# Kernel optimization log

Hardware: AMD Instinct MI355X
Metric: run time of the kernel (lower is better)

Reference implementation:

```python
import jax, jax.numpy as jnp
import numpy as np
import math


def _rope_2d(k, height, width):
    """Additive 2D sinusoidal position embedding. k: (B, N, D), N == height*width."""
    B, N, D = k.shape
    d_half = D // 2
    y_idx = jnp.arange(height, dtype=jnp.float32) / max(height - 1, 1)
    x_idx = jnp.arange(width, dtype=jnp.float32) / max(width - 1, 1)
    y_grid, x_grid = jnp.meshgrid(y_idx, x_idx, indexing='ij')
    y_flat = y_grid.reshape(-1)  # (N,)
    x_flat = x_grid.reshape(-1)
    freq = jnp.exp(jnp.arange(0, d_half, 2, dtype=jnp.float32) * (-(math.log(10000.0) / d_half)))

    def pos_half(flat, scale):
        ang = flat[:, None] * freq[None, :] * scale  # (N, ceil(d_half/2))
        p = jnp.zeros((N, d_half), dtype=jnp.float32)
        p = p.at[:, 0::2].set(jnp.sin(ang))
        n_odd = p[:, 1::2].shape[-1]
        p = p.at[:, 1::2].set(jnp.cos(ang[:, :n_odd]))
        return p

    pos_emb = jnp.concatenate([pos_half(y_flat, float(height)), pos_half(x_flat, float(width))], axis=-1)
    if pos_emb.shape[-1] < D:
        pos_emb = jnp.pad(pos_emb, ((0, 0), (0, D - pos_emb.shape[-1])))
    elif pos_emb.shape[-1] > D:
        pos_emb = pos_emb[:, :D]
    return k + pos_emb[None]


def setup_inputs() -> dict:
    key = jax.random.key(0)
    k1, k2, k3, k4 = jax.random.split(key, 4)
    B, N, dim = 2, 4096, 768
    num_heads, key_dim = 2, 8
    # xavier-uniform-like scales
    sq = math.sqrt(6.0 / (dim + num_heads * (key_dim + 1)))
    sk = math.sqrt(6.0 / (dim + key_dim))
    return {
        'query_tokens': jax.random.normal(k1, (B, N, dim), dtype=jnp.float32),
        'key_tokens': jax.random.normal(k2, (B, N, dim), dtype=jnp.float32),
        'Wq': jax.random.uniform(k3, (dim, num_heads * (key_dim + 1)), minval=-sq, maxval=sq, dtype=jnp.float32),
        'Wk': jax.random.uniform(k4, (dim, key_dim), minval=-sk, maxval=sk, dtype=jnp.float32),
        'spatial_bias': jnp.zeros((1, 1, 1), dtype=jnp.float32),
        'height': 64,
        'width': 64,
    }


def reference(query_tokens, key_tokens, Wq, Wk, spatial_bias, height, width):
    key_dim = Wk.shape[-1]
    num_heads = Wq.shape[-1] // (key_dim + 1)
    scale = key_dim ** (-0.5)
    B, N_q, _ = query_tokens.shape
    qw = (query_tokens @ Wq).reshape(B, N_q, num_heads, key_dim + 1)
    q = qw[..., :key_dim]          # (B, Nq, H, d)
    w = qw[..., -1]                # (B, Nq, H)
    k = key_tokens @ Wk            # (B, Nk, d)
    if height is not None and width is not None:
        k = _rope_2d(k, height, width)
    scores = jax.nn.relu(jnp.einsum('bqhd,bkd->bhqk', q, k) * scale)  # (B,H,Nq,Nk)
    index_scores = jnp.einsum('bqh,bhqk->bqk', w, scores)
    return index_scores + spatial_bias
```

## Files before the change

### kernel.cpp

```cpp
#include <hip/hip_runtime.h>
#include <math.h>

#define BB 2
#define NN 4096
#define DIM 768
#define QSTRIDE 20

__global__ __launch_bounds__(256) void qproj_kernel(const float* __restrict__ x,
                                                    const float* __restrict__ Wq,
                                                    float* __restrict__ qd) {
  const int lane = threadIdx.x & 63;
  const int pair = blockIdx.x * 4 + (threadIdx.x >> 6);
  const int row0 = pair * 2;
  const float* xr0 = x + (size_t)row0 * DIM;
  const float* xr1 = xr0 + DIM;

  float acc0[18], acc1[18];
#pragma unroll
  for (int c = 0; c < 18; ++c) { acc0[c] = 0.f; acc1[c] = 0.f; }

#pragma unroll
  for (int j = 0; j < DIM / 64; ++j) {
    const int i = lane + 64 * j;
    const float x0 = xr0[i];
    const float x1 = xr1[i];
    const float* wr = Wq + i * 18;
#pragma unroll
    for (int c = 0; c < 9; ++c) {
      const float2 w2 = *(const float2*)(wr + 2 * c);
      acc0[2 * c]     = fmaf(x0, w2.x, acc0[2 * c]);
      acc0[2 * c + 1] = fmaf(x0, w2.y, acc0[2 * c + 1]);
      acc1[2 * c]     = fmaf(x1, w2.x, acc1[2 * c]);
      acc1[2 * c + 1] = fmaf(x1, w2.y, acc1[2 * c + 1]);
    }
  }

#pragma unroll
  for (int off = 32; off >= 1; off >>= 1) {
#pragma unroll
    for (int c = 0; c < 18; ++c) {
      acc0[c] += __shfl_xor(acc0[c], off, 64);
      acc1[c] += __shfl_xor(acc1[c], off, 64);
    }
  }

  const int r = lane >> 5;
  const int l = lane & 31;
  if (l < 18) {
    int src;
    if (l < 8) src = l;
    else if (l < 16) src = l + 1;
    else if (l == 16) src = 8;
    else src = 17;
    float v = r ? acc1[0] : acc0[0];
#pragma unroll
    for (int c = 1; c < 18; ++c) {
      const float cand = r ? acc1[c] : acc0[c];
      v = (src == c) ? cand : v;
    }
    qd[(size_t)(row0 + r) * QSTRIDE + l] = v;
  }
}

__global__ __launch_bounds__(256) void kproj_kernel(const float* __restrict__ x,
                                                    const float* __restrict__ Wk,
                                                    const int* __restrict__ hp,
                                                    const int* __restrict__ wp,
                                                    float* __restrict__ kd) {
  const int lane = threadIdx.x & 63;
  const int pair = blockIdx.x * 4 + (threadIdx.x >> 6);
  const int row0 = pair * 2;
  const float* xr0 = x + (size_t)row0 * DIM;
  const float* xr1 = xr0 + DIM;

  float acc0[8], acc1[8];
#pragma unroll
  for (int c = 0; c < 8; ++c) { acc0[c] = 0.f; acc1[c] = 0.f; }

#pragma unroll
  for (int j = 0; j < DIM / 64; ++j) {
    const int i = lane + 64 * j;
    const float x0 = xr0[i];
    const float x1 = xr1[i];
    const float4 wa = *(const float4*)(Wk + i * 8);
    const float4 wb = *(const float4*)(Wk + i * 8 + 4);
    acc0[0] = fmaf(x0, wa.x, acc0[0]); acc0[1] = fmaf(x0, wa.y, acc0[1]);
    acc0[2] = fmaf(x0, wa.z, acc0[2]); acc0[3] = fmaf(x0, wa.w, acc0[3]);
    acc0[4] = fmaf(x0, wb.x, acc0[4]); acc0[5] = fmaf(x0, wb.y, acc0[5]);
    acc0[6] = fmaf(x0, wb.z, acc0[6]); acc0[7] = fmaf(x0, wb.w, acc0[7]);
    acc1[0] = fmaf(x1, wa.x, acc1[0]); acc1[1] = fmaf(x1, wa.y, acc1[1]);
    acc1[2] = fmaf(x1, wa.z, acc1[2]); acc1[3] = fmaf(x1, wa.w, acc1[3]);
    acc1[4] = fmaf(x1, wb.x, acc1[4]); acc1[5] = fmaf(x1, wb.y, acc1[5]);
    acc1[6] = fmaf(x1, wb.z, acc1[6]); acc1[7] = fmaf(x1, wb.w, acc1[7]);
  }

#pragma unroll
  for (int off = 32; off >= 1; off >>= 1) {
#pragma unroll
    for (int c = 0; c < 8; ++c) {
      acc0[c] += __shfl_xor(acc0[c], off, 64);
      acc1[c] += __shfl_xor(acc1[c], off, 64);
    }
  }

  const int r = lane >> 5;
  const int l = lane & 31;
  if (l < 8) {
    const int row = row0 + r;
    const int h = hp[0];
    const int w = wp[0];
    const int n = row % NN;
    const int yi = n / w;
    const int xi = n - yi * w;
    const int hd = (h - 1) > 1 ? (h - 1) : 1;
    const int wd = (w - 1) > 1 ? (w - 1) : 1;
    const float yv = (float)yi / (float)hd;
    const float xv = (float)xi / (float)wd;
    const float base = (l < 4) ? yv : xv;
    const float sc = (l < 4) ? (float)h : (float)w;
    const float fr = (l & 2) ? 0.01f : 1.0f;
    const float ang = base * fr * sc;
    const float pe = (l & 1) ? cosf(ang) : sinf(ang);
    float v = r ? acc1[0] : acc0[0];
#pragma unroll
    for (int c = 1; c < 8; ++c) {
      const float cand = r ? acc1[c] : acc0[c];
      v = (l == c) ? cand : v;
    }
    kd[(size_t)row * 8 + l] = v + pe;
  }
}

__device__ __forceinline__ float dot8(const float4 a, const float4 b,
                                      const float* __restrict__ k8) {
  float d = a.x * k8[0];
  d = fmaf(a.y, k8[1], d);
  d = fmaf(a.z, k8[2], d);
  d = fmaf(a.w, k8[3], d);
  d = fmaf(b.x, k8[4], d);
  d = fmaf(b.y, k8[5], d);
  d = fmaf(b.z, k8[6], d);
  d = fmaf(b.w, k8[7], d);
  return d;
}

__global__ __launch_bounds__(256) void scores_kernel(const float* __restrict__ qd,
                                                     const float* __restrict__ kd,
                                                     const float* __restrict__ bias,
                                                     float* __restrict__ out) {
  __shared__ float ks[64 * 9];
  __shared__ float qs[32 * QSTRIDE];

  const int tid = threadIdx.x;
  const int kb = blockIdx.x;
  const int qb = blockIdx.y;
  const int b  = blockIdx.z;

  if (tid < 128) {
    const float4 v = ((const float4*)(kd + ((size_t)b * NN + kb * 64) * 8))[tid];
    const int key = tid >> 1;
    const int off = (tid & 1) * 4;
    float* dst = ks + key * 9 + off;
    dst[0] = v.x; dst[1] = v.y; dst[2] = v.z; dst[3] = v.w;
  }
  if (tid < 160) {
    ((float4*)qs)[tid] = ((const float4*)(qd + ((size_t)b * NN + qb * 32) * QSTRIDE))[tid];
  }
  __syncthreads();

  const int tx = tid & 15;
  const int ty = tid >> 4;
  const float sb = bias[0];
  const float scale = 0.35355339059327373f;

  const int k0 = tx * 4;
  float kv[4][8];
#pragma unroll
  for (int i = 0; i < 4; ++i) {
    const float* kp = ks + (k0 + i) * 9;
#pragma unroll
    for (int d = 0; d < 8; ++d) kv[i][d] = kp[d];
  }

#pragma unroll
  for (int qi = 0; qi < 2; ++qi) {
    const int lq = ty * 2 + qi;
    const float* qp = qs + lq * QSTRIDE;
    const float4 a0 = *(const float4*)(qp);
    const float4 a1 = *(const float4*)(qp + 4);
    const float4 b0 = *(const float4*)(qp + 8);
    const float4 b1 = *(const float4*)(qp + 12);
    const float w0 = qp[16];
    const float w1 = qp[17];

    float4 res;
    float* r = (float*)&res;
#pragma unroll
    for (int i = 0; i < 4; ++i) {
      float d0 = dot8(a0, a1, kv[i]);
      float d1 = dot8(b0, b1, kv[i]);
      d0 = fmaxf(d0 * scale, 0.f);
      d1 = fmaxf(d1 * scale, 0.f);
      r[i] = fmaf(w0, d0, fmaf(w1, d1, sb));
    }

    const int q = qb * 32 + lq;
    float* op = out + ((size_t)b * NN + q) * (size_t)NN + (size_t)(kb * 64 + k0);
    *(float4*)op = res;
  }
}

extern "C" void kernel_launch(void* const* d_in, const int* in_sizes, int n_in,
                              void* d_out, int out_size, void* d_ws, size_t ws_size,
                              hipStream_t stream) {
  const float* qt = (const float*)d_in[0];
  const float* kt = (const float*)d_in[1];
  const float* Wq = (const float*)d_in[2];
  const float* Wk = (const float*)d_in[3];
  const float* sb = (const float*)d_in[4];
  const int* hp = (const int*)d_in[5];
  const int* wp = (const int*)d_in[6];

  float* qd = (float*)d_ws;
  float* kd = qd + (size_t)BB * NN * QSTRIDE;
  float* outp = (float*)d_out;

  qproj_kernel<<<BB * NN / 8, 256, 0, stream>>>(qt, Wq, qd);
  kproj_kernel<<<BB * NN / 8, 256, 0, stream>>>(kt, Wk, hp, wp, kd);
  scores_kernel<<<dim3(64, NN / 32, BB), 256, 0, stream>>>(qd, kd, sb, outp);
}
```

Before: 203.8 us.

## Merge projection kernels, widen key tile to 128, use nontemporal output stores

Fuses the q and k projection kernels into one launch that uses a 2D grid, removing one kernel launch. The scores kernel's key tile grows from 64 to 128, so each thread computes 8 keys and halves the number of blocks. Outputs are written with two nontemporal 16-byte stores to stream the 128MB result past the cache. The larger tile raises per-thread register use.

```diff
diff --git a/kernel.cpp b/kernel.cpp
--- a/kernel.cpp
+++ b/kernel.cpp
@@ -5,129 +5,131 @@
 #define NN 4096
 #define DIM 768
 #define QSTRIDE 20
-
-__global__ __launch_bounds__(256) void qproj_kernel(const float* __restrict__ x,
-                                                    const float* __restrict__ Wq,
-                                                    float* __restrict__ qd) {
+#define KT 128
+
+typedef float f32x4 __attribute__((ext_vector_type(4)));
+
+__global__ __launch_bounds__(256) void proj_kernel(const float* __restrict__ xq,
+                                                   const float* __restrict__ Wq,
+                                                   float* __restrict__ qd,
+                                                   const float* __restrict__ xk,
+                                                   const float* __restrict__ Wk,
+                                                   const int* __restrict__ hp,
+                                                   const int* __restrict__ wp,
+                                                   float* __restrict__ kd) {
   const int lane = threadIdx.x & 63;
   const int pair = blockIdx.x * 4 + (threadIdx.x >> 6);
   const int row0 = pair * 2;
-  const float* xr0 = x + (size_t)row0 * DIM;
-  const float* xr1 = xr0 + DIM;
-
-  float acc0[18], acc1[18];
-#pragma unroll
-  for (int c = 0; c < 18; ++c) { acc0[c] = 0.f; acc1[c] = 0.f; }
-
-#pragma unroll
-  for (int j = 0; j < DIM / 64; ++j) {
-    const int i = lane + 64 * j;
-    const float x0 = xr0[i];
-    const float x1 = xr1[i];
-    const float* wr = Wq + i * 18;
-#pragma unroll
-    for (int c = 0; c < 9; ++c) {
-      const float2 w2 = *(const float2*)(wr + 2 * c);
-      acc0[2 * c]     = fmaf(x0, w2.x, acc0[2 * c]);
-      acc0[2 * c + 1] = fmaf(x0, w2.y, acc0[2 * c + 1]);
-      acc1[2 * c]     = fmaf(x1, w2.x, acc1[2 * c]);
-      acc1[2 * c + 1] = fmaf(x1, w2.y, acc1[2 * c + 1]);
-    }
-  }
-
-#pragma unroll
-  for (int off = 32; off >= 1; off >>= 1) {
-#pragma unroll
-    for (int c = 0; c < 18; ++c) {
-      acc0[c] += __shfl_xor(acc0[c], off, 64);
-      acc1[c] += __shfl_xor(acc1[c], off, 64);
-    }
-  }
-
-  const int r = lane >> 5;
-  const int l = lane & 31;
-  if (l < 18) {
-    int src;
-    if (l < 8) src = l;
-    else if (l < 16) src = l + 1;
-    else if (l == 16) src = 8;
-    else src = 17;
-    float v = r ? acc1[0] : acc0[0];
-#pragma unroll
-    for (int c = 1; c < 18; ++c) {
-      const float cand = r ? acc1[c] : acc0[c];
-      v = (src == c) ? cand : v;
-    }
-    qd[(size_t)(row0 + r) * QSTRIDE + l] = v;
-  }
-}
-
-__global__ __launch_bounds__(256) void kproj_kernel(const float* __restrict__ x,
-                                                    const float* __restrict__ Wk,
-                                                    const int* __restrict__ hp,
-                                                    const int* __restrict__ wp,
-                                                    float* __restrict__ kd) {
-  const int lane = threadIdx.x & 63;
-  const int pair = blockIdx.x * 4 + (threadIdx.x >> 6);
-  const int row0 = pair * 2;
-  const float* xr0 = x + (size_t)row0 * DIM;
-  const float* xr1 = xr0 + DIM;
-
-  float acc0[8], acc1[8];
-#pragma unroll
-  for (int c = 0; c < 8; ++c) { acc0[c] = 0.f; acc1[c] = 0.f; }
-
-#pragma unroll
-  for (int j = 0; j < DIM / 64; ++j) {
-    const int i = lane + 64 * j;
-    const float x0 = xr0[i];
-    const float x1 = xr1[i];
-    const float4 wa = *(const float4*)(Wk + i * 8);
-    const float4 wb = *(const float4*)(Wk + i * 8 + 4);
-    acc0[0] = fmaf(x0, wa.x, acc0[0]); acc0[1] = fmaf(x0, wa.y, acc0[1]);
-    acc0[2] = fmaf(x0, wa.z, acc0[2]); acc0[3] = fmaf(x0, wa.w, acc0[3]);
-    acc0[4] = fmaf(x0, wb.x, acc0[4]); acc0[5] = fmaf(x0, wb.y, acc0[5]);
-    acc0[6] = fmaf(x0, wb.z, acc0[6]); acc0[7] = fmaf(x0, wb.w, acc0[7]);
-    acc1[0] = fmaf(x1, wa.x, acc1[0]); acc1[1] = fmaf(x1, wa.y, acc1[1]);
-    acc1[2] = fmaf(x1, wa.z, acc1[2]); acc1[3] = fmaf(x1, wa.w, acc1[3]);
-    acc1[4] = fmaf(x1, wb.x, acc1[4]); acc1[5] = fmaf(x1, wb.y, acc1[5]);
-    acc1[6] = fmaf(x1, wb.z, acc1[6]); acc1[7] = fmaf(x1, wb.w, acc1[7]);
-  }
-
-#pragma unroll
-  for (int off = 32; off >= 1; off >>= 1) {
-#pragma unroll
-    for (int c = 0; c < 8; ++c) {
-      acc0[c] += __shfl_xor(acc0[c], off, 64);
-      acc1[c] += __shfl_xor(acc1[c], off, 64);
-    }
-  }
-
-  const int r = lane >> 5;
-  const int l = lane & 31;
-  if (l < 8) {
-    const int row = row0 + r;
-    const int h = hp[0];
-    const int w = wp[0];
-    const int n = row % NN;
-    const int yi = n / w;
-    const int xi = n - yi * w;
-    const int hd = (h - 1) > 1 ? (h - 1) : 1;
-    const int wd = (w - 1) > 1 ? (w - 1) : 1;
-    const float yv = (float)yi / (float)hd;
-    const float xv = (float)xi / (float)wd;
-    const float base = (l < 4) ? yv : xv;
-    const float sc = (l < 4) ? (float)h : (float)w;
-    const float fr = (l & 2) ? 0.01f : 1.0f;
-    const float ang = base * fr * sc;
-    const float pe = (l & 1) ? cosf(ang) : sinf(ang);
-    float v = r ? acc1[0] : acc0[0];
-#pragma unroll
-    for (int c = 1; c < 8; ++c) {
-      const float cand = r ? acc1[c] : acc0[c];
-      v = (l == c) ? cand : v;
-    }
-    kd[(size_t)row * 8 + l] = v + pe;
+
+  if (blockIdx.y == 0) {
+    const float* xr0 = xq + (size_t)row0 * DIM;
+    const float* xr1 = xr0 + DIM;
+
+    float acc0[18], acc1[18];
+#pragma unroll
+    for (int c = 0; c < 18; ++c) { acc0[c] = 0.f; acc1[c] = 0.f; }
+
+#pragma unroll
+    for (int j = 0; j < DIM / 64; ++j) {
+      const int i = lane + 64 * j;
+      const float x0 = xr0[i];
+      const float x1 = xr1[i];
+      const float* wr = Wq + i * 18;
+#pragma unroll
+      for (int c = 0; c < 9; ++c) {
+        const float2 w2 = *(const float2*)(wr + 2 * c);
+        acc0[2 * c]     = fmaf(x0, w2.x, acc0[2 * c]);
+        acc0[2 * c + 1] = fmaf(x0, w2.y, acc0[2 * c + 1]);
+        acc1[2 * c]     = fmaf(x1, w2.x, acc1[2 * c]);
+        acc1[2 * c + 1] = fmaf(x1, w2.y, acc1[2 * c + 1]);
+      }
+    }
+
+#pragma unroll
+    for (int off = 32; off >= 1; off >>= 1) {
+#pragma unroll
+      for (int c = 0; c < 18; ++c) {
+        acc0[c] += __shfl_xor(acc0[c], off, 64);
+        acc1[c] += __shfl_xor(acc1[c], off, 64);
+      }
+    }
+
+    const int r = lane >> 5;
+    const int l = lane & 31;
+    if (l < 18) {
+      int src;
+      if (l < 8) src = l;
+      else if (l < 16) src = l + 1;
+      else if (l == 16) src = 8;
+      else src = 17;
+      float v = r ? acc1[0] : acc0[0];
+#pragma unroll
+      for (int c = 1; c < 18; ++c) {
+        const float cand = r ? acc1[c] : acc0[c];
+        v = (src == c) ? cand : v;
+      }
+      qd[(size_t)(row0 + r) * QSTRIDE + l] = v;
+    }
+  } else {
+    const float* xr0 = xk + (size_t)row0 * DIM;
+    const float* xr1 = xr0 + DIM;
+
+    float acc0[8], acc1[8];
+#pragma unroll
+    for (int c = 0; c < 8; ++c) { acc0[c] = 0.f; acc1[c] = 0.f; }
+
+#pragma unroll
+    for (int j = 0; j < DIM / 64; ++j) {
+      const int i = lane + 64 * j;
+      const float x0 = xr0[i];
+      const float x1 = xr1[i];
+      const float4 wa = *(const float4*)(Wk + i * 8);
+      const float4 wb = *(const float4*)(Wk + i * 8 + 4);
+      acc0[0] = fmaf(x0, wa.x, acc0[0]); acc0[1] = fmaf(x0, wa.y, acc0[1]);
+      acc0[2] = fmaf(x0, wa.z, acc0[2]); acc0[3] = fmaf(x0, wa.w, acc0[3]);
+      acc0[4] = fmaf(x0, wb.x, acc0[4]); acc0[5] = fmaf(x0, wb.y, acc0[5]);
+      acc0[6] = fmaf(x0, wb.z, acc0[6]); acc0[7] = fmaf(x0, wb.w, acc0[7]);
+      acc1[0] = fmaf(x1, wa.x, acc1[0]); acc1[1] = fmaf(x1, wa.y, acc1[1]);
+      acc1[2] = fmaf(x1, wa.z, acc1[2]); acc1[3] = fmaf(x1, wa.w, acc1[3]);
+      acc1[4] = fmaf(x1, wb.x, acc1[4]); acc1[5] = fmaf(x1, wb.y, acc1[5]);
+      acc1[6] = fmaf(x1, wb.z, acc1[6]); acc1[7] = fmaf(x1, wb.w, acc1[7]);
+    }
+
+#pragma unroll
+    for (int off = 32; off >= 1; off >>= 1) {
+#pragma unroll
+      for (int c = 0; c < 8; ++c) {
+        acc0[c] += __shfl_xor(acc0[c], off, 64);
+        acc1[c] += __shfl_xor(acc1[c], off, 64);
+      }
+    }
+
+    const int r = lane >> 5;
+    const int l = lane & 31;
+    if (l < 8) {
+      const int row = row0 + r;
+      const int h = hp[0];
+      const int w = wp[0];
+      const int n = row % NN;
+      const int yi = n / w;
+      const int xi = n - yi * w;
+      const int hd = (h - 1) > 1 ? (h - 1) : 1;
+      const int wd = (w - 1) > 1 ? (w - 1) : 1;
+      const float yv = (float)yi / (float)hd;
+      const float xv = (float)xi / (float)wd;
+      const float base = (l < 4) ? yv : xv;
+      const float sc = (l < 4) ? (float)h : (float)w;
+      const float fr = (l & 2) ? 0.01f : 1.0f;
+      const float ang = base * fr * sc;
+      const float pe = (l & 1) ? cosf(ang) : sinf(ang);
+      float v = r ? acc1[0] : acc0[0];
+#pragma unroll
+      for (int c = 1; c < 8; ++c) {
+        const float cand = r ? acc1[c] : acc0[c];
+        v = (l == c) ? cand : v;
+      }
+      kd[(size_t)row * 8 + l] = v + pe;
+    }
   }
 }
 
@@ -148,7 +150,7 @@
                                                      const float* __restrict__ kd,
                                                      const float* __restrict__ bias,
                                                      float* __restrict__ out) {
-  __shared__ float ks[64 * 9];
+  __shared__ float ks[KT * 9];
   __shared__ float qs[32 * QSTRIDE];
 
   const int tid = threadIdx.x;
@@ -156,8 +158,8 @@
   const int qb = blockIdx.y;
   const int b  = blockIdx.z;
 
-  if (tid < 128) {
-    const float4 v = ((const float4*)(kd + ((size_t)b * NN + kb * 64) * 8))[tid];
+  {
+    const float4 v = ((const float4*)(kd + ((size_t)b * NN + kb * KT) * 8))[tid];
     const int key = tid >> 1;
     const int off = (tid & 1) * 4;
     float* dst = ks + key * 9 + off;
@@ -173,10 +175,10 @@
   const float sb = bias[0];
   const float scale = 0.35355339059327373f;
 
-  const int k0 = tx * 4;
-  float kv[4][8];
-#pragma unroll
-  for (int i = 0; i < 4; ++i) {
+  const int k0 = tx * 8;
+  float kv[8][8];
+#pragma unroll
+  for (int i = 0; i < 8; ++i) {
     const float* kp = ks + (k0 + i) * 9;
 #pragma unroll
     for (int d = 0; d < 8; ++d) kv[i][d] = kp[d];
@@ -193,10 +195,10 @@
     const float w0 = qp[16];
     const float w1 = qp[17];
 
-    float4 res;
-    float* r = (float*)&res;
-#pragma unroll
-    for (int i = 0; i < 4; ++i) {
+    f32x4 res[2];
+    float* r = (float*)res;
+#pragma unroll
+    for (int i = 0; i < 8; ++i) {
       float d0 = dot8(a0, a1, kv[i]);
       float d1 = dot8(b0, b1, kv[i]);
       d0 = fmaxf(d0 * scale, 0.f);
@@ -205,8 +207,9 @@
     }
 
     const int q = qb * 32 + lq;
-    float* op = out + ((size_t)b * NN + q) * (size_t)NN + (size_t)(kb * 64 + k0);
-    *(float4*)op = res;
+    float* op = out + ((size_t)b * NN + q) * (size_t)NN + (size_t)(kb * KT + k0);
+    __builtin_nontemporal_store(res[0], (f32x4*)op);
+    __builtin_nontemporal_store(res[1], (f32x4*)(op + 4));
   }
 }
 
@@ -225,7 +228,6 @@
   float* kd = qd + (size_t)BB * NN * QSTRIDE;
   float* outp = (float*)d_out;
 
-  qproj_kernel<<<BB * NN / 8, 256, 0, stream>>>(qt, Wq, qd);
-  kproj_kernel<<<BB * NN / 8, 256, 0, stream>>>(kt, Wk, hp, wp, kd);
-  scores_kernel<<<dim3(64, NN / 32, BB), 256, 0, stream>>>(qd, kd, sb, outp);
-}
+  proj_kernel<<<dim3(BB * NN / 8, 2), 256, 0, stream>>>(qt, Wq, qd, kt, Wk, hp, wp, kd);
+  scores_kernel<<<dim3(NN / KT, NN / 32, BB), 256, 0, stream>>>(qd, kd, sb, outp);
+}
```

After: 210.7 us. +3.4%, slower.
